# Performance work log

Hardware: AMD Instinct MI355X
Metric: run time of the kernel (lower is better)

The kernel has to match this reference:

```python
import jax, jax.numpy as jnp
import numpy as np
from jax import lax

HIDDEN = 1024
STATE = 64
BATCH = 16
SEQ = 2048
DT_MIN, DT_MAX = 0.001, 0.1


def setup_inputs() -> dict:
    key = jax.random.key(0)
    k = jax.random.split(key, 6)
    x = jax.random.normal(k[0], (BATCH, SEQ, HIDDEN), dtype=jnp.float32)
    A = jax.random.normal(k[1], (STATE, STATE), dtype=jnp.float32) * 0.01
    B = jax.random.normal(k[2], (STATE, HIDDEN), dtype=jnp.float32) * 0.01
    C = jax.random.normal(k[3], (HIDDEN, STATE), dtype=jnp.float32) * 0.01
    D = jnp.ones((HIDDEN,), dtype=jnp.float32)
    log_dt = jax.random.uniform(k[4], (HIDDEN,), dtype=jnp.float32) * (
        np.log(DT_MAX) - np.log(DT_MIN)
    ) + np.log(DT_MIN)
    return {"x": x, "A": A, "B": B, "C": C, "D": D, "log_dt": log_dt}


def reference(x, A, B, C, D, log_dt):
    # x: (B, T, H)
    dt = jnp.exp(log_dt)                                  # (H,)
    A_bar = jax.scipy.linalg.expm(A * dt.mean())          # (N, N)
    B_bar = B * dt[None, :]                               # (N, H)
    # Precompute input injection for all timesteps: (B, T, N)
    u = jnp.einsum("bth,nh->btn", x, B_bar)

    def step(state, u_t):
        # state: (B, N); u_t: (B, N)
        state = state @ A_bar.T + u_t
        return state, state

    init = jnp.zeros((x.shape[0], A.shape[0]), dtype=x.dtype)
    _, states = lax.scan(step, init, jnp.swapaxes(u, 0, 1))  # (T, B, N)
    states = jnp.swapaxes(states, 0, 1)                      # (B, T, N)
    return jnp.einsum("btn,hn->bth", states, C) + D * x
```

## Files before the change

kernel.cpp:

```cpp
#include <hip/hip_runtime.h>


#define H   1024
#define NS  64
#define NB  16
#define TT  2048
#define LCH 64
#define KCH 32

typedef __attribute__((ext_vector_type(8))) short bf16x8;
typedef __attribute__((ext_vector_type(4))) float f32x4;
typedef __attribute__((ext_vector_type(2))) unsigned int u32x2;

#define WS_ABAR 0
#define WS_AL   4096
#define WS_F    8192
#define WS_P    40960
#define WS_U    73728
#define WS_S    2170880
#define WS_BBF  8192
#define WS_CBF  3219456

__device__ __forceinline__ unsigned short f2bf(float x) {
  union { float f; unsigned u; } v; v.f = x;
  unsigned r = (v.u + 0x7FFFu + ((v.u >> 16) & 1u)) >> 16;
  return (unsigned short)r;
}

__device__ __forceinline__ bf16x8 packbf8(f32x4 a, f32x4 b) {
  bf16x8 r;
  r[0] = (short)f2bf(a[0]); r[1] = (short)f2bf(a[1]);
  r[2] = (short)f2bf(a[2]); r[3] = (short)f2bf(a[3]);
  r[4] = (short)f2bf(b[0]); r[5] = (short)f2bf(b[1]);
  r[6] = (short)f2bf(b[2]); r[7] = (short)f2bf(b[3]);
  return r;
}

__device__ __forceinline__ u32x2 packbf4(f32x4 v) {
  u32x2 r;
  r[0] = (unsigned)f2bf(v[0]) | ((unsigned)f2bf(v[1]) << 16);
  r[1] = (unsigned)f2bf(v[2]) | ((unsigned)f2bf(v[3]) << 16);
  return r;
}

__device__ __forceinline__ f32x4 mfma16(bf16x8 a, bf16x8 b, f32x4 c) {
  return __builtin_amdgcn_mfma_f32_16x16x32_bf16(a, b, c, 0, 0, 0);
}

__global__ __launch_bounds__(256) void k0(const float* Bm, const float* Cm,
                                          const float* ldt, float* ws) {
  short* Bbf = (short*)(ws + WS_BBF);
  short* Cbf = (short*)(ws + WS_CBF);
  const int idx = (blockIdx.x * 256 + threadIdx.x) * 4;
  f32x4 b = *(const f32x4*)(Bm + idx);
  f32x4 l = *(const f32x4*)(ldt + (idx & (H - 1)));
  f32x4 bb;
  for (int j = 0; j < 4; ++j) bb[j] = b[j] * expf(l[j]);
  *(u32x2*)&Bbf[idx] = packbf4(bb);
  f32x4 c = *(const f32x4*)(Cm + idx);
  *(u32x2*)&Cbf[idx] = packbf4(c);
}

__device__ void prep_block(const float* Ain, const float* ldt, float* ws, int which) {
  __shared__ float Mb[64 * 68];
  __shared__ short Tl[64 * 72];
  const int lane = threadIdx.x;
  const int cq = lane >> 4, cl = lane & 15;

  float s = 0.f;
  for (int j = 0; j < 16; ++j) s += expf(ldt[lane + j * 64]);
  for (int off = 32; off; off >>= 1) s += __shfl_down(s, off);
  float dtm = __shfl(s, 0) * (1.0f / 1024.0f);
  float scale = which ? dtm * (float)LCH : dtm;

  for (int idx = lane; idx < 4096; idx += 64) {
    int r = idx >> 6, c = idx & 63;
    float v = Ain[idx] * scale;
    Mb[c * 68 + r] = v;
    Tl[r * 72 + c] = (short)f2bf(v);
  }

  float E[16][4];
  for (int mt = 0; mt < 4; ++mt)
    for (int nt = 0; nt < 4; ++nt)
      for (int r = 0; r < 4; ++r) {
        int row = mt * 16 + cq * 4 + r, col = nt * 16 + cl;
        E[mt * 4 + nt][r] = (row == col ? 1.f : 0.f) + Ain[row * 64 + col] * scale;
      }

  __asm volatile("s_waitcnt lgkmcnt(0)" ::: "memory");

  for (int it = 2; it <= 12; ++it) {
    bf16x8 af[4][2];
    for (int mt = 0; mt < 4; ++mt)
      for (int kh = 0; kh < 2; ++kh)
        af[mt][kh] = *(const bf16x8*)&Tl[(mt * 16 + cl) * 72 + kh * 32 + cq * 8];
    float inv = 1.0f / (float)it;
    bf16x8 bfr[4][2];
    for (int nt = 0; nt < 4; ++nt)
      for (int kh = 0; kh < 2; ++kh) {
        const float* p = &Mb[(nt * 16 + cl) * 68 + kh * 32 + cq * 8];
        f32x4 a = *(const f32x4*)p;
        f32x4 b = *(const f32x4*)(p + 4);
        bfr[nt][kh] = packbf8(a * inv, b * inv);
      }
    f32x4 zero = {0.f, 0.f, 0.f, 0.f};
    f32x4 acc[16];
    for (int i = 0; i < 16; ++i) acc[i] = zero;
    for (int mt = 0; mt < 4; ++mt)
      for (int nt = 0; nt < 4; ++nt) {
        acc[mt * 4 + nt] = mfma16(af[mt][0], bfr[nt][0], acc[mt * 4 + nt]);
        acc[mt * 4 + nt] = mfma16(af[mt][1], bfr[nt][1], acc[mt * 4 + nt]);
      }
    __asm volatile("s_waitcnt lgkmcnt(0)" ::: "memory");
    for (int mt = 0; mt < 4; ++mt)
      for (int nt = 0; nt < 4; ++nt)
        for (int r = 0; r < 4; ++r) {
          float t = acc[mt * 4 + nt][r];
          E[mt * 4 + nt][r] += t;
          Tl[(mt * 16 + cq * 4 + r) * 72 + nt * 16 + cl] = (short)f2bf(t);
        }
    __asm volatile("s_waitcnt lgkmcnt(0)" ::: "memory");
  }

  float* dst = ws + (which ? WS_AL : WS_ABAR);
  for (int mt = 0; mt < 4; ++mt)
    for (int nt = 0; nt < 4; ++nt)
      for (int r = 0; r < 4; ++r)
        dst[(mt * 16 + cq * 4 + r) * 64 + nt * 16 + cl] = E[mt * 4 + nt][r];
}

__device__ void gemm_u(const float* x, const float* ws, float* u2, int bid) {
  const short* Bbf = (const short*)(ws + WS_BBF);
  const int tid = threadIdx.x;
  const int wid = tid >> 6, lane = tid & 63;
  const int cq = lane >> 4, cl = lane & 15;
  const int bt0 = bid * 64 + wid * 16;

  const float* xr = x + (long)(bt0 + cl) * H + cq * 8;
  const short* br = Bbf + cq * 8;

  f32x4 zero = {0.f, 0.f, 0.f, 0.f};
  f32x4 acc[4];
  for (int i = 0; i < 4; ++i) acc[i] = zero;

#pragma unroll 4
  for (int ks = 0; ks < 32; ++ks) {
    const int k0 = ks * 32;
    f32x4 xa = *(const f32x4*)(xr + k0);
    f32x4 xb = *(const f32x4*)(xr + k0 + 4);
    bf16x8 af = packbf8(xa, xb);
    for (int nt = 0; nt < 4; ++nt) {
      bf16x8 bf = *(const bf16x8*)(br + (nt * 16 + cl) * H + k0);
      acc[nt] = mfma16(af, bf, acc[nt]);
    }
  }

  for (int nt = 0; nt < 4; ++nt)
    for (int r = 0; r < 4; ++r) {
      int obt = bt0 + cq * 4 + r;
      int t = obt & (TT - 1), b = obt >> 11;
      u2[(long)(t * 16 + b) * 64 + nt * 16 + cl] = acc[nt][r];
    }
}

__global__ __launch_bounds__(256) void k1(const float* x, const float* Ain,
                                          const float* ldt, float* ws) {
  if (blockIdx.x < 2) {
    if (threadIdx.x < 64) prep_block(Ain, ldt, ws, blockIdx.x);
    return;
  }
  gemm_u(x, ws, ws + WS_U, blockIdx.x - 2);
}

__device__ __forceinline__ void load_RF(const float* Amat, bf16x8 Rf[4][2], int cq, int cl) {
  for (int mt = 0; mt < 4; ++mt)
    for (int kh = 0; kh < 2; ++kh) {
      int m = mt * 16 + cl;
      int kb = kh * 32 + cq * 8;
      f32x4 v0 = *(const f32x4*)&Amat[m * 64 + kb];
      f32x4 v1 = *(const f32x4*)&Amat[m * 64 + kb + 4];
      for (int j = 0; j < 4; ++j) {
        if (m == kb + j) v0[j] -= 1.f;
        if (m == kb + 4 + j) v1[j] -= 1.f;
      }
      Rf[mt][kh] = packbf8(v0, v1);
    }
}

__device__ __forceinline__ void scan_step(f32x4 Z[4], const bf16x8 Rf[4][2], short* Zl,
                                          const f32x4 U[4], int cq, int cl) {
  for (int t = 0; t < 4; ++t)
    *(u32x2*)&Zl[cl * 72 + t * 16 + cq * 4] = packbf4(Z[t]);
  __asm volatile("s_waitcnt lgkmcnt(0)" ::: "memory");
  bf16x8 zf0 = *(const bf16x8*)&Zl[cl * 72 + cq * 8];
  bf16x8 zf1 = *(const bf16x8*)&Zl[cl * 72 + 32 + cq * 8];
  for (int t = 0; t < 4; ++t) Z[t] += U[t];
  for (int mt = 0; mt < 4; ++mt) {
    Z[mt] = mfma16(Rf[mt][0], zf0, Z[mt]);
    Z[mt] = mfma16(Rf[mt][1], zf1, Z[mt]);
  }
}

__global__ __launch_bounds__(64) void scan_local_k(float* ws) {
  const float* Abar = ws + WS_ABAR;
  const float* u2 = ws + WS_U;
  float* F = ws + WS_F;
  __shared__ short Zl[16 * 72];
  const int lane = threadIdx.x, cq = lane >> 4, cl = lane & 15;
  const int c = blockIdx.x;
  bf16x8 Rf[4][2];
  load_RF(Abar, Rf, cq, cl);
  f32x4 zero = {0.f, 0.f, 0.f, 0.f};
  f32x4 Z[4], U[4], Un[4];
  for (int t = 0; t < 4; ++t) Z[t] = zero;
  const float* ub = u2 + (long)c * LCH * 1024 + cl * 64 + cq * 4;
  for (int t = 0; t < 4; ++t) U[t] = *(const f32x4*)(ub + t * 16);
  for (int ti = 0; ti < LCH; ++ti) {
    const float* un = ub + (ti + 1) * 1024;
    for (int t = 0; t < 4; ++t) Un[t] = *(const f32x4*)(un + t * 16);
    scan_step(Z, Rf, Zl, U, cq, cl);
    for (int t = 0; t < 4; ++t) U[t] = Un[t];
  }
  for (int t = 0; t < 4; ++t)
    *(f32x4*)&F[(long)c * 1024 + cl * 64 + t * 16 + cq * 4] = Z[t];
}

__global__ __launch_bounds__(64) void scan_chunks_k(float* ws) {
  const float* AL = ws + WS_AL;
  const float* F = ws + WS_F;
  float* P = ws + WS_P;
  __shared__ short Zl[16 * 72];
  const int lane = threadIdx.x, cq = lane >> 4, cl = lane & 15;
  bf16x8 Rf[4][2];
  load_RF(AL, Rf, cq, cl);
  f32x4 zero = {0.f, 0.f, 0.f, 0.f};
  f32x4 Z[4], U[4];
  for (int t = 0; t < 4; ++t) Z[t] = zero;
  for (int c = 0; c < KCH; ++c) {
    long off = (long)c * 1024 + cl * 64 + cq * 4;
    for (int t = 0; t < 4; ++t) *(f32x4*)&P[off + t * 16] = Z[t];
    for (int t = 0; t < 4; ++t) U[t] = *(const f32x4*)&F[off + t * 16];
    scan_step(Z, Rf, Zl, U, cq, cl);
  }
}

__global__ __launch_bounds__(64) void scan_final_k(float* ws) {
  const float* Abar = ws + WS_ABAR;
  const float* u2 = ws + WS_U;
  const float* P = ws + WS_P;
  short* S2bf = (short*)(ws + WS_S);
  __shared__ short Zl[16 * 72];
  const int lane = threadIdx.x, cq = lane >> 4, cl = lane & 15;
  const int c = blockIdx.x;
  bf16x8 Rf[4][2];
  load_RF(Abar, Rf, cq, cl);
  f32x4 Z[4], U[4], Un[4];
  long poff = (long)c * 1024 + cl * 64 + cq * 4;
  for (int t = 0; t < 4; ++t) Z[t] = *(const f32x4*)&P[poff + t * 16];
  const float* ub = u2 + (long)c * LCH * 1024 + cl * 64 + cq * 4;
  short* sb = S2bf + (long)c * LCH * 1024 + cl * 64 + cq * 4;
  for (int t = 0; t < 4; ++t) U[t] = *(const f32x4*)(ub + t * 16);
  for (int ti = 0; ti < LCH; ++ti) {
    const float* un = ub + (ti + 1) * 1024;
    for (int t = 0; t < 4; ++t) Un[t] = *(const f32x4*)(un + t * 16);
    scan_step(Z, Rf, Zl, U, cq, cl);
    short* so = sb + ti * 1024;
    for (int t = 0; t < 4; ++t) *(u32x2*)(so + t * 16) = packbf4(Z[t]);
    for (int t = 0; t < 4; ++t) U[t] = Un[t];
  }
}

__global__ __launch_bounds__(256) void out_proj_k(const float* ws, const float* Dv,
                                                  const float* x, float* out) {
  const short* Sbf = (const short*)(ws + WS_S);
  const short* Cbf = (const short*)(ws + WS_CBF);
  const int tid = threadIdx.x;
  const int wid = tid >> 6, lane = tid & 63;
  const int cq = lane >> 4, cl = lane & 15;
  const int bid = blockIdx.x;
  const int bt0 = (bid & 511) * 64 + wid * 16;
  const int h0 = (bid >> 9) * 128;

  const int abt = bt0 + cl;
  const int at = abt & (TT - 1), ab = abt >> 11;
  const short* sr = Sbf + (long)(at * 16 + ab) * 64 + cq * 8;
  bf16x8 a0 = *(const bf16x8*)(sr);
  bf16x8 a1 = *(const bf16x8*)(sr + 32);

#pragma unroll
  for (int nt = 0; nt < 8; ++nt) {
    const int h = h0 + nt * 16 + cl;
    const short* cr = Cbf + (long)h * 64 + cq * 8;
    bf16x8 b0 = *(const bf16x8*)(cr);
    bf16x8 b1 = *(const bf16x8*)(cr + 32);
    f32x4 acc = {0.f, 0.f, 0.f, 0.f};
    acc = mfma16(a0, b0, acc);
    acc = mfma16(a1, b1, acc);
    const float d = Dv[h];
    for (int r = 0; r < 4; ++r) {
      long obt = bt0 + cq * 4 + r;
      long idx = obt * H + h;
      out[idx] = acc[r] + d * x[idx];
    }
  }
}

extern "C" void kernel_launch(void* const* d_in, const int* in_sizes, int n_in,
                              void* d_out, int out_size, void* d_ws, size_t ws_size,
                              hipStream_t stream) {
  const float* x = (const float*)d_in[0];
  const float* A = (const float*)d_in[1];
  const float* Bm = (const float*)d_in[2];
  const float* Cm = (const float*)d_in[3];
  const float* Dv = (const float*)d_in[4];
  const float* ldt = (const float*)d_in[5];
  float* out = (float*)d_out;
  float* ws = (float*)d_ws;

  k0<<<dim3(64), dim3(256), 0, stream>>>(Bm, Cm, ldt, ws);
  k1<<<dim3(2 + 512), dim3(256), 0, stream>>>(x, A, ldt, ws);
  scan_local_k<<<dim3(KCH), dim3(64), 0, stream>>>(ws);
  scan_chunks_k<<<dim3(1), dim3(64), 0, stream>>>(ws);
  scan_final_k<<<dim3(KCH), dim3(64), 0, stream>>>(ws);
  out_proj_k<<<dim3(4096), dim3(256), 0, stream>>>(ws, Dv, x, out);
}
```

Before: 507.0 us.

## Fuse chunk-carry scan into final scan, prefetch inputs, vectorize stores via swapped MFMA operands

Moves the matrix-exponential prep blocks into the weight-conversion kernel so the input-projection GEMM runs alone. The GEMM now prefetches x two k-steps ahead, and its MFMA operands are swapped so each lane writes a contiguous f32x4 of u instead of scattered scalars. The single-block chunk-carry scan kernel is removed: each final-scan block recomputes its own prefix over earlier chunk states, which costs redundant work in later blocks but saves one launch. The local and final scans use a triple-buffered u prefetch. The output projection also swaps operands so the x loads and out stores become 16-byte vectors.

Result: faster. 490.9 us (-3.2%).

```diff
diff --git a/kernel.cpp b/kernel.cpp
--- a/kernel.cpp
+++ b/kernel.cpp
@@ -2,8 +2,6 @@
 
 
 #define H   1024
-#define NS  64
-#define NB  16
 #define TT  2048
 #define LCH 64
 #define KCH 32
@@ -45,20 +43,6 @@
 
 __device__ __forceinline__ f32x4 mfma16(bf16x8 a, bf16x8 b, f32x4 c) {
   return __builtin_amdgcn_mfma_f32_16x16x32_bf16(a, b, c, 0, 0, 0);
-}
-
-__global__ __launch_bounds__(256) void k0(const float* Bm, const float* Cm,
-                                          const float* ldt, float* ws) {
-  short* Bbf = (short*)(ws + WS_BBF);
-  short* Cbf = (short*)(ws + WS_CBF);
-  const int idx = (blockIdx.x * 256 + threadIdx.x) * 4;
-  f32x4 b = *(const f32x4*)(Bm + idx);
-  f32x4 l = *(const f32x4*)(ldt + (idx & (H - 1)));
-  f32x4 bb;
-  for (int j = 0; j < 4; ++j) bb[j] = b[j] * expf(l[j]);
-  *(u32x2*)&Bbf[idx] = packbf4(bb);
-  f32x4 c = *(const f32x4*)(Cm + idx);
-  *(u32x2*)&Cbf[idx] = packbf4(c);
 }
 
 __device__ void prep_block(const float* Ain, const float* ldt, float* ws, int which) {
@@ -130,12 +114,31 @@
         dst[(mt * 16 + cq * 4 + r) * 64 + nt * 16 + cl] = E[mt * 4 + nt][r];
 }
 
-__device__ void gemm_u(const float* x, const float* ws, float* u2, int bid) {
+__global__ __launch_bounds__(256) void k0(const float* Bm, const float* Cm,
+                                          const float* Ain, const float* ldt, float* ws) {
+  if (blockIdx.x >= 64) {
+    if (threadIdx.x < 64) prep_block(Ain, ldt, ws, blockIdx.x - 64);
+    return;
+  }
+  short* Bbf = (short*)(ws + WS_BBF);
+  short* Cbf = (short*)(ws + WS_CBF);
+  const int idx = (blockIdx.x * 256 + threadIdx.x) * 4;
+  f32x4 b = *(const f32x4*)(Bm + idx);
+  f32x4 l = *(const f32x4*)(ldt + (idx & (H - 1)));
+  f32x4 bb;
+  for (int j = 0; j < 4; ++j) bb[j] = b[j] * expf(l[j]);
+  *(u32x2*)&Bbf[idx] = packbf4(bb);
+  f32x4 c = *(const f32x4*)(Cm + idx);
+  *(u32x2*)&Cbf[idx] = packbf4(c);
+}
+
+__global__ __launch_bounds__(256) void k1(const float* x, float* ws) {
   const short* Bbf = (const short*)(ws + WS_BBF);
+  float* u2 = ws + WS_U;
   const int tid = threadIdx.x;
   const int wid = tid >> 6, lane = tid & 63;
   const int cq = lane >> 4, cl = lane & 15;
-  const int bt0 = bid * 64 + wid * 16;
+  const int bt0 = (blockIdx.x * 4 + wid) * 16;
 
   const float* xr = x + (long)(bt0 + cl) * H + cq * 8;
   const short* br = Bbf + cq * 8;
@@ -144,33 +147,31 @@
   f32x4 acc[4];
   for (int i = 0; i < 4; ++i) acc[i] = zero;
 
-#pragma unroll 4
+  f32x4 pxa[2], pxb[2];
+  pxa[0] = *(const f32x4*)(xr);       pxb[0] = *(const f32x4*)(xr + 4);
+  pxa[1] = *(const f32x4*)(xr + 32);  pxb[1] = *(const f32x4*)(xr + 36);
+
+#pragma unroll
   for (int ks = 0; ks < 32; ++ks) {
-    const int k0 = ks * 32;
-    f32x4 xa = *(const f32x4*)(xr + k0);
-    f32x4 xb = *(const f32x4*)(xr + k0 + 4);
-    bf16x8 af = packbf8(xa, xb);
+    f32x4 xa = pxa[ks & 1], xb = pxb[ks & 1];
+    if (ks < 30) {
+      pxa[ks & 1] = *(const f32x4*)(xr + (ks + 2) * 32);
+      pxb[ks & 1] = *(const f32x4*)(xr + (ks + 2) * 32 + 4);
+    }
+    bf16x8 bfx = packbf8(xa, xb);
+#pragma unroll
     for (int nt = 0; nt < 4; ++nt) {
-      bf16x8 bf = *(const bf16x8*)(br + (nt * 16 + cl) * H + k0);
-      acc[nt] = mfma16(af, bf, acc[nt]);
+      bf16x8 bfb = *(const bf16x8*)(br + (nt * 16 + cl) * H + ks * 32);
+      acc[nt] = mfma16(bfb, bfx, acc[nt]);
     }
   }
 
+  const int bt = bt0 + cl;
+  const int t = bt & (TT - 1), b = bt >> 11;
+  float* ur = u2 + (long)(t * 16 + b) * 64 + cq * 4;
+#pragma unroll
   for (int nt = 0; nt < 4; ++nt)
-    for (int r = 0; r < 4; ++r) {
-      int obt = bt0 + cq * 4 + r;
-      int t = obt & (TT - 1), b = obt >> 11;
-      u2[(long)(t * 16 + b) * 64 + nt * 16 + cl] = acc[nt][r];
-    }
-}
-
-__global__ __launch_bounds__(256) void k1(const float* x, const float* Ain,
-                                          const float* ldt, float* ws) {
-  if (blockIdx.x < 2) {
-    if (threadIdx.x < 64) prep_block(Ain, ldt, ws, blockIdx.x);
-    return;
-  }
-  gemm_u(x, ws, ws + WS_U, blockIdx.x - 2);
+    *(f32x4*)(ur + nt * 16) = acc[nt];
 }
 
 __device__ __forceinline__ void load_RF(const float* Amat, bf16x8 Rf[4][2], int cq, int cl) {
@@ -203,71 +204,64 @@
 }
 
 __global__ __launch_bounds__(64) void scan_local_k(float* ws) {
-  const float* Abar = ws + WS_ABAR;
   const float* u2 = ws + WS_U;
   float* F = ws + WS_F;
   __shared__ short Zl[16 * 72];
   const int lane = threadIdx.x, cq = lane >> 4, cl = lane & 15;
   const int c = blockIdx.x;
   bf16x8 Rf[4][2];
-  load_RF(Abar, Rf, cq, cl);
+  load_RF(ws + WS_ABAR, Rf, cq, cl);
   f32x4 zero = {0.f, 0.f, 0.f, 0.f};
-  f32x4 Z[4], U[4], Un[4];
+  f32x4 Z[4], Ub[3][4];
   for (int t = 0; t < 4; ++t) Z[t] = zero;
   const float* ub = u2 + (long)c * LCH * 1024 + cl * 64 + cq * 4;
-  for (int t = 0; t < 4; ++t) U[t] = *(const f32x4*)(ub + t * 16);
+  for (int t = 0; t < 4; ++t) Ub[0][t] = *(const f32x4*)(ub + t * 16);
+  for (int t = 0; t < 4; ++t) Ub[1][t] = *(const f32x4*)(ub + 1024 + t * 16);
+#pragma unroll
   for (int ti = 0; ti < LCH; ++ti) {
-    const float* un = ub + (ti + 1) * 1024;
-    for (int t = 0; t < 4; ++t) Un[t] = *(const f32x4*)(un + t * 16);
-    scan_step(Z, Rf, Zl, U, cq, cl);
-    for (int t = 0; t < 4; ++t) U[t] = Un[t];
+    const float* un = ub + (ti + 2) * 1024;
+    for (int t = 0; t < 4; ++t) Ub[(ti + 2) % 3][t] = *(const f32x4*)(un + t * 16);
+    scan_step(Z, Rf, Zl, Ub[ti % 3], cq, cl);
   }
   for (int t = 0; t < 4; ++t)
     *(f32x4*)&F[(long)c * 1024 + cl * 64 + t * 16 + cq * 4] = Z[t];
 }
 
-__global__ __launch_bounds__(64) void scan_chunks_k(float* ws) {
-  const float* AL = ws + WS_AL;
-  const float* F = ws + WS_F;
-  float* P = ws + WS_P;
-  __shared__ short Zl[16 * 72];
-  const int lane = threadIdx.x, cq = lane >> 4, cl = lane & 15;
-  bf16x8 Rf[4][2];
-  load_RF(AL, Rf, cq, cl);
-  f32x4 zero = {0.f, 0.f, 0.f, 0.f};
-  f32x4 Z[4], U[4];
-  for (int t = 0; t < 4; ++t) Z[t] = zero;
-  for (int c = 0; c < KCH; ++c) {
-    long off = (long)c * 1024 + cl * 64 + cq * 4;
-    for (int t = 0; t < 4; ++t) *(f32x4*)&P[off + t * 16] = Z[t];
-    for (int t = 0; t < 4; ++t) U[t] = *(const f32x4*)&F[off + t * 16];
-    scan_step(Z, Rf, Zl, U, cq, cl);
-  }
-}
-
 __global__ __launch_bounds__(64) void scan_final_k(float* ws) {
-  const float* Abar = ws + WS_ABAR;
   const float* u2 = ws + WS_U;
-  const float* P = ws + WS_P;
   short* S2bf = (short*)(ws + WS_S);
   __shared__ short Zl[16 * 72];
   const int lane = threadIdx.x, cq = lane >> 4, cl = lane & 15;
   const int c = blockIdx.x;
   bf16x8 Rf[4][2];
-  load_RF(Abar, Rf, cq, cl);
-  f32x4 Z[4], U[4], Un[4];
-  long poff = (long)c * 1024 + cl * 64 + cq * 4;
-  for (int t = 0; t < 4; ++t) Z[t] = *(const f32x4*)&P[poff + t * 16];
+  f32x4 zero = {0.f, 0.f, 0.f, 0.f};
+  f32x4 Z[4];
+  for (int t = 0; t < 4; ++t) Z[t] = zero;
+
+  if (c > 0) {
+    load_RF(ws + WS_AL, Rf, cq, cl);
+    const float* Fb = ws + WS_F;
+    f32x4 U[4];
+    for (int j = 0; j < c; ++j) {
+      const float* fb = Fb + (long)j * 1024 + cl * 64 + cq * 4;
+      for (int t = 0; t < 4; ++t) U[t] = *(const f32x4*)(fb + t * 16);
+      scan_step(Z, Rf, Zl, U, cq, cl);
+    }
+  }
+
+  load_RF(ws + WS_ABAR, Rf, cq, cl);
+  f32x4 Ub[3][4];
   const float* ub = u2 + (long)c * LCH * 1024 + cl * 64 + cq * 4;
   short* sb = S2bf + (long)c * LCH * 1024 + cl * 64 + cq * 4;
-  for (int t = 0; t < 4; ++t) U[t] = *(const f32x4*)(ub + t * 16);
+  for (int t = 0; t < 4; ++t) Ub[0][t] = *(const f32x4*)(ub + t * 16);
+  for (int t = 0; t < 4; ++t) Ub[1][t] = *(const f32x4*)(ub + 1024 + t * 16);
+#pragma unroll
   for (int ti = 0; ti < LCH; ++ti) {
-    const float* un = ub + (ti + 1) * 1024;
-    for (int t = 0; t < 4; ++t) Un[t] = *(const f32x4*)(un + t * 16);
-    scan_step(Z, Rf, Zl, U, cq, cl);
+    const float* un = ub + (ti + 2) * 1024;
+    for (int t = 0; t < 4; ++t) Ub[(ti + 2) % 3][t] = *(const f32x4*)(un + t * 16);
+    scan_step(Z, Rf, Zl, Ub[ti % 3], cq, cl);
     short* so = sb + ti * 1024;
     for (int t = 0; t < 4; ++t) *(u32x2*)(so + t * 16) = packbf4(Z[t]);
-    for (int t = 0; t < 4; ++t) U[t] = Un[t];
   }
 }
 
@@ -285,24 +279,24 @@
   const int abt = bt0 + cl;
   const int at = abt & (TT - 1), ab = abt >> 11;
   const short* sr = Sbf + (long)(at * 16 + ab) * 64 + cq * 8;
-  bf16x8 a0 = *(const bf16x8*)(sr);
-  bf16x8 a1 = *(const bf16x8*)(sr + 32);
+  bf16x8 s0 = *(const bf16x8*)(sr);
+  bf16x8 s1 = *(const bf16x8*)(sr + 32);
+  const long row = (long)abt * H;
 
 #pragma unroll
   for (int nt = 0; nt < 8; ++nt) {
-    const int h = h0 + nt * 16 + cl;
-    const short* cr = Cbf + (long)h * 64 + cq * 8;
-    bf16x8 b0 = *(const bf16x8*)(cr);
-    bf16x8 b1 = *(const bf16x8*)(cr + 32);
+    const int ht = h0 + nt * 16;
+    const short* cr = Cbf + (long)(ht + cl) * 64 + cq * 8;
+    bf16x8 c0 = *(const bf16x8*)(cr);
+    bf16x8 c1 = *(const bf16x8*)(cr + 32);
     f32x4 acc = {0.f, 0.f, 0.f, 0.f};
-    acc = mfma16(a0, b0, acc);
-    acc = mfma16(a1, b1, acc);
-    const float d = Dv[h];
-    for (int r = 0; r < 4; ++r) {
-      long obt = bt0 + cq * 4 + r;
-      long idx = obt * H + h;
-      out[idx] = acc[r] + d * x[idx];
-    }
+    acc = mfma16(c0, s0, acc);
+    acc = mfma16(c1, s1, acc);
+    const long idx = row + ht + cq * 4;
+    f32x4 xv = *(const f32x4*)(x + idx);
+    f32x4 dv = *(const f32x4*)(Dv + ht + cq * 4);
+    for (int j = 0; j < 4; ++j) acc[j] += dv[j] * xv[j];
+    *(f32x4*)(out + idx) = acc;
   }
 }
 
@@ -318,10 +312,9 @@
   float* out = (float*)d_out;
   float* ws = (float*)d_ws;
 
-  k0<<<dim3(64), dim3(256), 0, stream>>>(Bm, Cm, ldt, ws);
-  k1<<<dim3(2 + 512), dim3(256), 0, stream>>>(x, A, ldt, ws);
+  k0<<<dim3(66), dim3(256), 0, stream>>>(Bm, Cm, A, ldt, ws);
+  k1<<<dim3(512), dim3(256), 0, stream>>>(x, ws);
   scan_local_k<<<dim3(KCH), dim3(64), 0, stream>>>(ws);
-  scan_chunks_k<<<dim3(1), dim3(64), 0, stream>>>(ws);
   scan_final_k<<<dim3(KCH), dim3(64), 0, stream>>>(ws);
   out_proj_k<<<dim3(4096), dim3(256), 0, stream>>>(ws, Dv, x, out);
 }
```
